# Kernel optimization log

Measured on AMD Instinct MI355X. Metric: run time of the kernel, lower is better.

The kernel has to match this reference:

```python
import jax, jax.numpy as jnp
import numpy as np
from jax import lax

B, T_IN, T_OUT = 32, 256, 500
N_MEL, ENC_DIM = 80, 512
ATT_RNN, DEC_RNN, PRENET, ATT_DIM = 1024, 1024, 256, 128
LOC_F, LOC_K = 32, 31
P_ATT_DROP, P_DEC_DROP = 0.1, 0.1


def setup_inputs() -> dict:
    key = jax.random.key(0)
    ks = jax.random.split(key, 24)
    rn = lambda k, s, sc=0.02: jax.random.normal(k, s, dtype=jnp.float32) * sc
    inp = {}
    inp['memory'] = jax.random.normal(ks[0], (B, T_IN, ENC_DIM), dtype=jnp.float32)
    inp['decoder_inputs'] = jax.random.normal(ks[1], (B, N_MEL, T_OUT), dtype=jnp.float32)
    inp['memory_lengths'] = jax.random.randint(ks[2], (B,), T_IN // 2, T_IN + 1)
    inp['prenet_w1'] = rn(ks[3], (PRENET, N_MEL))
    inp['prenet_w2'] = rn(ks[4], (PRENET, PRENET))
    inp['att_w_ih'] = rn(ks[5], (4 * ATT_RNN, PRENET + ENC_DIM))
    inp['att_w_hh'] = rn(ks[6], (4 * ATT_RNN, ATT_RNN))
    inp['att_b_ih'] = jnp.zeros((4 * ATT_RNN,), jnp.float32)
    inp['att_b_hh'] = jnp.zeros((4 * ATT_RNN,), jnp.float32)
    inp['query_w'] = rn(ks[7], (ATT_DIM, ATT_RNN))
    inp['memory_w'] = rn(ks[8], (ATT_DIM, ENC_DIM))
    inp['v_w'] = rn(ks[9], (1, ATT_DIM))
    inp['loc_conv_w'] = rn(ks[10], (LOC_F, 2, LOC_K))
    inp['loc_dense_w'] = rn(ks[11], (ATT_DIM, LOC_F))
    inp['dec_w_ih'] = rn(ks[12], (4 * DEC_RNN, ATT_RNN + ENC_DIM))
    inp['dec_w_hh'] = rn(ks[13], (4 * DEC_RNN, DEC_RNN))
    inp['dec_b_ih'] = jnp.zeros((4 * DEC_RNN,), jnp.float32)
    inp['dec_b_hh'] = jnp.zeros((4 * DEC_RNN,), jnp.float32)
    inp['proj_w'] = rn(ks[14], (N_MEL, DEC_RNN + ENC_DIM))
    inp['proj_b'] = jnp.zeros((N_MEL,), jnp.float32)
    inp['gate_w'] = rn(ks[15], (1, DEC_RNN + ENC_DIM))
    inp['gate_b'] = jnp.zeros((1,), jnp.float32)
    return inp


def _lstm_cell(x, h, c, w_ih, w_hh, b_ih, b_hh):
    gates = x @ w_ih.T + b_ih + h @ w_hh.T + b_hh
    i, f, g, o = jnp.split(gates, 4, axis=-1)
    c2 = jax.nn.sigmoid(f) * c + jax.nn.sigmoid(i) * jnp.tanh(g)
    h2 = jax.nn.sigmoid(o) * jnp.tanh(c2)
    return h2, c2


def _dropout_masks():
    # deterministic dropout masks (training=True semantics), keep-prob scaled
    kd = jax.random.key(1)
    k1, k2, k3, k4 = jax.random.split(kd, 4)
    m1 = jax.random.bernoulli(k1, 0.5, (T_OUT + 1, B, PRENET)).astype(jnp.float32) / 0.5
    m2 = jax.random.bernoulli(k2, 0.5, (T_OUT + 1, B, PRENET)).astype(jnp.float32) / 0.5
    ma = jax.random.bernoulli(k3, 1 - P_ATT_DROP, (T_OUT, B, ATT_RNN)).astype(jnp.float32) / (1 - P_ATT_DROP)
    md = jax.random.bernoulli(k4, 1 - P_DEC_DROP, (T_OUT, B, DEC_RNN)).astype(jnp.float32) / (1 - P_DEC_DROP)
    return m1, m2, ma, md


def _decode(memory, decoder_inputs, memory_lengths, prenet_w1, prenet_w2,
            att_w_ih, att_w_hh, att_b_ih, att_b_hh, query_w, memory_w, v_w,
            loc_conv_w, loc_dense_w, dec_w_ih, dec_w_hh, dec_b_ih, dec_b_hh,
            proj_w, proj_b, gate_w, gate_b):
    pm1, pm2, att_drop, dec_drop = _dropout_masks()
    processed_memory = jnp.einsum('bte,ae->bta', memory, memory_w)  # (B,T_in,128)
    pad_mask = jnp.arange(T_IN)[None, :] >= memory_lengths[:, None]  # True = padded

    # teacher-forced decoder inputs: (B,n_mel,T) -> (T,B,n_mel), prepend go frame
    dec_in = jnp.transpose(decoder_inputs, (2, 0, 1))
    dec_in = jnp.concatenate([jnp.zeros((1, B, N_MEL), dec_in.dtype), dec_in], 0)
    # prenet (relu + dropout p=0.5, always training)
    x = jax.nn.relu(dec_in @ prenet_w1.T) * pm1
    x = jax.nn.relu(x @ prenet_w2.T) * pm2
    prenet_out = x[:T_OUT]  # (T,B,256)

    pad = (LOC_K - 1) // 2

    def attention(att_h, aw, aw_cum):
        pq = att_h @ query_w.T  # (B,128)
        awc = jnp.stack([aw, aw_cum], axis=1)  # (B,2,T_in)
        loc = lax.conv_general_dilated(awc, loc_conv_w, (1,), [(pad, pad)],
                                       dimension_numbers=('NCH', 'OIH', 'NCH'))  # (B,32,T_in)
        loc = jnp.einsum('bft,af->bta', loc, loc_dense_w)  # (B,T_in,128)
        energies = jnp.tanh(pq[:, None, :] + loc + processed_memory) @ v_w[0]  # (B,T_in)
        energies = jnp.where(pad_mask, -jnp.inf, energies)
        w = jax.nn.softmax(energies, axis=1)
        ctx = jnp.einsum('bt,bte->be', w, memory)  # (B,512)
        return ctx, w

    def step(carry, xs):
        ah, ac, dh, dc, aw, aw_cum, ctx = carry
        pn, adm, ddm = xs
        cell_in = jnp.concatenate([pn, ctx], axis=-1)  # (B,768)
        ah, ac = _lstm_cell(cell_in, ah, ac, att_w_ih, att_w_hh, att_b_ih, att_b_hh)
        ah = ah * adm
        ctx, aw = attention(ah, aw, aw_cum)
        aw_cum = aw_cum + aw
        din = jnp.concatenate([ah, ctx], axis=-1)  # (B,1536)
        dh, dc = _lstm_cell(din, dh, dc, dec_w_ih, dec_w_hh, dec_b_ih, dec_b_hh)
        dh = dh * ddm
        dhac = jnp.concatenate([dh, ctx], axis=-1)  # (B,1536)
        mel = dhac @ proj_w.T + proj_b  # (B,80)
        gate = (dhac @ gate_w.T + gate_b)[:, 0]  # (B,)
        return (ah, ac, dh, dc, aw, aw_cum, ctx), (mel, gate, aw)

    z = lambda d: jnp.zeros((B, d), jnp.float32)
    init = (z(ATT_RNN), z(ATT_RNN), z(DEC_RNN), z(DEC_RNN),
            jnp.zeros((B, T_IN), jnp.float32), jnp.zeros((B, T_IN), jnp.float32), z(ENC_DIM))
    _, (mels, gates, aligns) = lax.scan(step, init, (prenet_out, att_drop, dec_drop))

    mel_outputs = jnp.transpose(mels, (1, 2, 0))   # (B, n_mel, T_out)
    gate_outputs = gates.T                          # (B, T_out)
    alignments = jnp.transpose(aligns, (1, 0, 2))   # (B, T_out, T_in)
    return mel_outputs, gate_outputs, alignments


def reference(memory, decoder_inputs, memory_lengths, prenet_w1, prenet_w2,
              att_w_ih, att_w_hh, att_b_ih, att_b_hh, query_w, memory_w, v_w,
              loc_conv_w, loc_dense_w, dec_w_ih, dec_w_hh, dec_b_ih, dec_b_hh,
              proj_w, proj_b, gate_w, gate_b):
    return _decode(memory, decoder_inputs, memory_lengths, prenet_w1, prenet_w2,
                   att_w_ih, att_w_hh, att_b_ih, att_b_hh, query_w, memory_w, v_w,
                   loc_conv_w, loc_dense_w, dec_w_ih, dec_w_hh, dec_b_ih, dec_b_hh,
                   proj_w, proj_b, gate_w, gate_b)
```

## Files before the change

kernel.cpp:

```cpp
#include <hip/hip_runtime.h>
#include <math.h>
#include <string.h>

#define TOUT 500
#define AOFF 1296000
#define GOFF 1280000
#define TF_BITS_XOR 1

typedef float f32x4 __attribute__((ext_vector_type(4)));
typedef short bf16x8 __attribute__((ext_vector_type(8)));
typedef unsigned short ushort4_t __attribute__((ext_vector_type(4)));
typedef unsigned u32x4 __attribute__((ext_vector_type(4)));

struct Params {
  const float *memory, *dec_in, *pw1, *pw2, *awih, *awhh, *abih, *abhh;
  const float *qw, *mw, *vw, *lcw, *ldw, *dwih, *dwhh, *dbih, *dbhh;
  const float *pjw, *pjb, *gw, *gb;
  const int* mlen;
  float* out;
  unsigned short *ahb0, *ahb1, *dhb0, *dhb1, *ctxb0, *ctxb1;
  unsigned *slots;
  unsigned *flags;
  float *x1, *w1t, *w2t, *mwt, *ldwt, *ba, *bd;
  unsigned short *pre_bf, *pm_bf, *mem_bf, *qw_bf, *wpa, *wpd;
  unsigned *mma, *mmd, *mm1, *mm2;
};

__host__ __device__ inline void tf_block(unsigned k0, unsigned k1, unsigned x0, unsigned x1,
                                         unsigned& o0, unsigned& o1) {
  unsigned ks2 = k0 ^ k1 ^ 0x1BD11BDAu;
  x0 += k0; x1 += k1;
#define TFR(r) { x0 += x1; x1 = (x1 << r) | (x1 >> (32 - r)); x1 ^= x0; }
  TFR(13) TFR(15) TFR(26) TFR(6)
  x0 += k1;  x1 += ks2 + 1u;
  TFR(17) TFR(29) TFR(16) TFR(24)
  x0 += ks2; x1 += k0 + 2u;
  TFR(13) TFR(15) TFR(26) TFR(6)
  x0 += k0;  x1 += k1 + 3u;
  TFR(17) TFR(29) TFR(16) TFR(24)
  x0 += k1;  x1 += ks2 + 4u;
  TFR(13) TFR(15) TFR(26) TFR(6)
  x0 += ks2; x1 += k0 + 5u;
#undef TFR
  o0 = x0; o1 = x1;
}

__device__ inline float sigf(float x) { return 1.f / (1.f + __expf(-x)); }
__device__ inline float tanh_fast(float x) {
  float ax = fabsf(x);
  float t = __expf(-2.f * ax);
  float r = (1.f - t) / (1.f + t);
  return copysignf(r, x);
}
__device__ inline unsigned short f2bf(float f) {
  unsigned u = __float_as_uint(f);
  unsigned r = (u + 0x7FFFu + ((u >> 16) & 1u)) >> 16;
  return (unsigned short)r;
}
__device__ inline float bf2f(unsigned short u) {
  return __uint_as_float((unsigned)u << 16);
}

__device__ inline unsigned long long ld_coh64(const void* ptr) {
  return __hip_atomic_load((unsigned long long*)ptr, __ATOMIC_RELAXED, __HIP_MEMORY_SCOPE_SYSTEM);
}
__device__ inline unsigned ld_coh32(const unsigned* ptr) {
  return __hip_atomic_load(ptr, __ATOMIC_RELAXED, __HIP_MEMORY_SCOPE_SYSTEM);
}
__device__ inline void st_coh32(unsigned* ptr, unsigned v) {
  __hip_atomic_store(ptr, v, __ATOMIC_RELAXED, __HIP_MEMORY_SCOPE_SYSTEM);
}

template<bool COH>
__device__ __forceinline__ u32x4 ld16(const void* ptr) {
  u32x4 r;
  if constexpr (COH)
    asm volatile("global_load_dwordx4 %0, %1, off sc0 sc1" : "=v"(r) : "v"(ptr));
  else
    asm volatile("global_load_dwordx4 %0, %1, off" : "=v"(r) : "v"(ptr));
  return r;
}

#define LD4(p) (*(const float4*)(p))

__global__ void maskgen_kernel(Params p, unsigned k1a, unsigned k1b, unsigned k2a, unsigned k2b,
                               unsigned k3a, unsigned k3b, unsigned k4a, unsigned k4b) {
  int t = blockIdx.x * 256 + threadIdx.x;
  unsigned ka, kb; unsigned* dst; float pp;
  if (t < 512000)       { ka = k3a; kb = k3b; dst = p.mma; pp = 0.9f; }
  else if (t < 1024000) { t -= 512000;  ka = k4a; kb = k4b; dst = p.mmd; pp = 0.9f; }
  else if (t < 1152256) { t -= 1024000; ka = k1a; kb = k1b; dst = p.mm1; pp = 0.5f; }
  else if (t < 1280512) { t -= 1152256; ka = k2a; kb = k2b; dst = p.mm2; pp = 0.5f; }
  else return;
  unsigned word = 0u;
  for (int i = 0; i < 32; ++i) {
    unsigned o0, o1;
    tf_block(ka, kb, 0u, (unsigned)t * 32u + (unsigned)i, o0, o1);
#if TF_BITS_XOR
    unsigned bits = o0 ^ o1;
#else
    unsigned bits = o0;
#endif
    unsigned fb = (bits >> 9) | 0x3f800000u;
    float u = __uint_as_float(fb) - 1.0f;
    if (u < pp) word |= (1u << i);
  }
  dst[t] = word;
}

__global__ void prep_misc(Params p) {
  int i = blockIdx.x * 256 + threadIdx.x;
  if (i < 20480) { int k = i >> 8, u = i & 255; p.w1t[i] = p.pw1[u * 80 + k]; return; }
  i -= 20480;
  if (i < 65536) { int k = i >> 8, u = i & 255; p.w2t[i] = p.pw2[u * 256 + k]; return; }
  i -= 65536;
  if (i < 65536) { int k = i >> 7, a = i & 127; p.mwt[i] = p.mw[a * 512 + k]; return; }
  i -= 65536;
  if (i < 131072) { p.qw_bf[i] = f2bf(p.qw[i]); return; }
  i -= 131072;
  if (i < 4096) { int f = i >> 7, a = i & 127; p.ldwt[i] = p.ldw[a * 32 + f]; return; }
  i -= 4096;
  if (i < 4096) { int col = (i & 3) * 1024 + (i >> 2); p.ba[i] = p.abih[col] + p.abhh[col]; return; }
  i -= 4096;
  if (i < 4096) { int col = (i & 3) * 1024 + (i >> 2); p.bd[i] = p.dbih[col] + p.dbhh[col]; return; }
  i -= 4096;
  if (i < 4194304) { p.mem_bf[i] = f2bf(p.memory[i]); return; }
}

__global__ void pack_att(Params p) {
  int idx = blockIdx.x * 256 + threadIdx.x;
  if (idx >= 256 * 56 * 64) return;
  int l = idx & 63;
  int c = (idx >> 6) % 56;
  int T = idx / (56 * 64);
  int n = T * 16 + (l & 15);
  int col = (n & 3) * 1024 + (n >> 2);
  int kb = c * 32 + 8 * (l >> 4);
  bf16x8 v;
#pragma unroll
  for (int j = 0; j < 8; ++j) {
    int k = kb + j;
    float f = (k < 768) ? p.awih[(size_t)col * 768 + k] : p.awhh[(size_t)col * 1024 + k - 768];
    v[j] = (short)f2bf(f);
  }
  *(bf16x8*)(p.wpa + (size_t)idx * 8) = v;
}
__global__ void pack_dec(Params p) {
  int idx = blockIdx.x * 256 + threadIdx.x;
  if (idx >= 256 * 80 * 64) return;
  int l = idx & 63;
  int c = (idx >> 6) % 80;
  int T = idx / (80 * 64);
  int n = T * 16 + (l & 15);
  int col = (n & 3) * 1024 + (n >> 2);
  int kb = c * 32 + 8 * (l >> 4);
  bf16x8 v;
#pragma unroll
  for (int j = 0; j < 8; ++j) {
    int k = kb + j;
    float f = (k < 1536) ? p.dwih[(size_t)col * 1536 + k] : p.dwhh[(size_t)col * 1024 + k - 1536];
    v[j] = (short)f2bf(f);
  }
  *(bf16x8*)(p.wpd + (size_t)idx * 8) = v;
}

__global__ void prenet1_kernel(Params p) {
  __shared__ float din[8][80];
  int wg = blockIdx.x, tid = threadIdx.x;
  int r0 = wg * 8;
  for (int idx = tid; idx < 8 * 80; idx += 256) {
    int j = idx / 80, kk = idx % 80;
    int r = r0 + j; int t = r >> 5, b = r & 31;
    din[j][kk] = (t == 0) ? 0.f : p.dec_in[(size_t)b * 40000 + (size_t)kk * 500 + (t - 1)];
  }
  __syncthreads();
  float acc[8] = {0,0,0,0,0,0,0,0};
  for (int k = 0; k < 80; ++k) {
    float wv = p.w1t[k * 256 + tid];
#pragma unroll
    for (int j = 0; j < 8; ++j) acc[j] += din[j][k] * wv;
  }
  for (int j = 0; j < 8; ++j) {
    int r = r0 + j;
    unsigned e = (unsigned)r * 256u + tid;
    float mv = ((p.mm1[e >> 5] >> (e & 31)) & 1u) ? 2.0f : 0.0f;
    p.x1[(size_t)r * 256 + tid] = fmaxf(acc[j], 0.f) * mv;
  }
}
__global__ void prenet2_kernel(Params p) {
  __shared__ float rows[8][256];
  int wg = blockIdx.x, tid = threadIdx.x;
  int r0 = wg * 8;
  for (int idx = tid; idx < 8 * 256; idx += 256) {
    int j = idx >> 8, kk = idx & 255;
    rows[j][kk] = p.x1[(size_t)(r0 + j) * 256 + kk];
  }
  __syncthreads();
  float acc[8] = {0,0,0,0,0,0,0,0};
  for (int k = 0; k < 256; ++k) {
    float wv = p.w2t[k * 256 + tid];
#pragma unroll
    for (int j = 0; j < 8; ++j) acc[j] += rows[j][k] * wv;
  }
  for (int j = 0; j < 8; ++j) {
    int r = r0 + j;
    unsigned e = (unsigned)r * 256u + tid;
    float mv = ((p.mm2[e >> 5] >> (e & 31)) & 1u) ? 2.0f : 0.0f;
    p.pre_bf[(size_t)r * 256 + tid] = f2bf(fmaxf(acc[j], 0.f) * mv);
  }
}

__global__ void pm_kernel(Params p) {
  __shared__ float mrows[16][512];
  int wg = blockIdx.x;
  int b = wg >> 4, tc = wg & 15;
  int tid = threadIdx.x;
  int t0 = tc * 16;
  for (int idx = tid; idx < 16 * 512; idx += 128) {
    int i = idx >> 9, k = idx & 511;
    mrows[i][k] = p.memory[((size_t)b * 256 + t0 + i) * 512 + k];
  }
  __syncthreads();
  float acc[16];
#pragma unroll
  for (int i = 0; i < 16; ++i) acc[i] = 0.f;
  for (int k = 0; k < 512; ++k) {
    float wv = p.mwt[k * 128 + tid];
#pragma unroll
    for (int i = 0; i < 16; ++i) acc[i] += mrows[i][k] * wv;
  }
  for (int i = 0; i < 16; ++i)
    p.pm_bf[((size_t)b * 256 + t0 + i) * 128 + tid] = f2bf(acc[i]);
}

template<int LEN, bool COH>
struct Seg {
  static constexpr int CPR = LEN / 8;
  static constexpr int N = (32 * CPR) / 512;
  u32x4 r[N];
  __device__ __forceinline__ void load(const unsigned short* src, int srcStride, int tid) {
#pragma unroll
    for (int i = 0; i < N; ++i) {
      int idx = tid + i * 512;
      int b = idx / CPR, c = idx % CPR;
      r[i] = ld16<COH>(src + (size_t)b * srcStride + c * 8);
    }
  }
  __device__ __forceinline__ void store(unsigned short* dst, int dstOff, int dstStride, int tid) {
#pragma unroll
    for (int i = 0; i < N; ++i) {
      int idx = tid + i * 512;
      int b = idx / CPR, c = idx % CPR;
      *(u32x4*)(dst + b * dstStride + dstOff + c * 8) = r[i];
    }
  }
};

__device__ __forceinline__ void drain_vm() {
  asm volatile("s_waitcnt vmcnt(0)" ::: "memory");
  __builtin_amdgcn_sched_barrier(0);
}

#define MFMA_BF16(a, b, c) __builtin_amdgcn_mfma_f32_16x16x32_bf16(a, b, c, 0, 0, 0)

template<int NC, int CPW, int P0J, bool ATT>
__device__ __forceinline__ void gemm_tile2(const Params& p, const bf16x8* bfa, const bf16x8* bfb,
                                           int lane, int v, int s,
                                           const unsigned short* ctxb_prev,
                                           const unsigned short* ahb_prev,
                                           const unsigned short* dhb_prev2,
                                           unsigned short* Abuf, float* pl, int tid) {
  const int arow = lane & 15;
  const int kgrp = (lane >> 4) * 8;
  f32x4 acc00 = {0,0,0,0}, acc01 = {0,0,0,0}, acc10 = {0,0,0,0}, acc11 = {0,0,0,0};

  const int RS0 = ATT ? 776 : 1288;
  if (ATT) {
    Seg<256, false> s0; Seg<512, true> s1;
    s0.load(p.pre_bf + (size_t)s * 32 * 256, 256, tid);
    s1.load(ctxb_prev, 512, tid);
    drain_vm();
    s0.store(Abuf, 0, RS0, tid);
    s1.store(Abuf, 256, RS0, tid);
  } else {
    Seg<1024, true> s0; Seg<256, true> s1;
    s0.load(ahb_prev, 1024, tid);
    s1.load(ctxb_prev, 512, tid);
    drain_vm();
    s0.store(Abuf, 0, RS0, tid);
    s1.store(Abuf, 1024, RS0, tid);
  }
  __syncthreads();
#pragma unroll
  for (int j = 0; j < P0J; ++j) {
    const int kc = (v + 8 * j) * 32;
    const int off = arow * RS0 + kc + kgrp;
    bf16x8 a0 = *(const bf16x8*)&Abuf[off];
    bf16x8 a1 = *(const bf16x8*)&Abuf[off + 16 * RS0];
    acc00 = MFMA_BF16(a0, bfa[j], acc00);
    acc01 = MFMA_BF16(a1, bfa[j], acc01);
    acc10 = MFMA_BF16(a0, bfb[j], acc10);
    acc11 = MFMA_BF16(a1, bfb[j], acc11);
  }
  __syncthreads();

  const int RS1 = ATT ? 1032 : 1288;
  if (ATT) {
    Seg<1024, true> s0;
    s0.load(ahb_prev, 1024, tid);
    drain_vm();
    s0.store(Abuf, 0, RS1, tid);
  } else {
    Seg<256, true> s0; Seg<1024, true> s1;
    s0.load(ctxb_prev + 256, 512, tid);
    s1.load(dhb_prev2, 1024, tid);
    drain_vm();
    s0.store(Abuf, 0, RS1, tid);
    s1.store(Abuf, 256, RS1, tid);
  }
  __syncthreads();
  const int K1 = ATT ? 768 : 1280;
#pragma unroll
  for (int j = P0J; j < CPW; ++j) {
    const int kc = (v + 8 * j) * 32 - K1;
    const int off = arow * RS1 + kc + kgrp;
    bf16x8 a0 = *(const bf16x8*)&Abuf[off];
    bf16x8 a1 = *(const bf16x8*)&Abuf[off + 16 * RS1];
    acc00 = MFMA_BF16(a0, bfa[j], acc00);
    acc01 = MFMA_BF16(a1, bfa[j], acc01);
    acc10 = MFMA_BF16(a0, bfb[j], acc10);
    acc11 = MFMA_BF16(a1, bfb[j], acc11);
  }
  __syncthreads();

  const int po = (lane & 15) * 17 + (lane >> 4) * 4;
#pragma unroll
  for (int j = 0; j < 4; ++j) {
    pl[v * 1088 +   0 + po + j] = acc00[j];
    pl[v * 1088 + 272 + po + j] = acc01[j];
    pl[v * 1088 + 544 + po + j] = acc10[j];
    pl[v * 1088 + 816 + po + j] = acc11[j];
  }
}

template<bool MASTER>
__device__ __forceinline__ void gbar(const Params& p, int wg, int tid, unsigned bargen) {
  __syncthreads();
  if (MASTER) {
    if (tid == 0) st_coh32(p.slots + wg * 32, bargen);
    for (;;) {
      int ok = 1;
      if (tid < 256) ok = (ld_coh32(p.slots + tid * 32) >= bargen) ? 1 : 0;
      if (__syncthreads_count(ok) == 512) break;
      __builtin_amdgcn_s_sleep(1);
    }
    if (tid < 8) st_coh32(p.flags + tid * 32, bargen);
  } else {
    if (tid == 0) {
      st_coh32(p.slots + wg * 32, bargen);
      while (ld_coh32(p.flags + (wg & 7) * 32) < bargen)
        __builtin_amdgcn_s_sleep(2);
    }
    __syncthreads();
  }
}

template<bool IS_ATT, bool MASTER>
__device__ __forceinline__ void run_scan(const Params& p, int wg, int tid,
                                         unsigned short* Abuf, float* pl, float* gates,
                                         float* cst, float* aw_l, float* awc_l, float* sm,
                                         unsigned short* ahst, unsigned short* cxst,
                                         unsigned short* hst) {
  const int lane = tid & 63;
  const int v = tid >> 6;
  constexpr int NC  = IS_ATT ? 56 : 80;
  constexpr int CPW = IS_ATT ? 7 : 10;
  constexpr int P0J = IS_ATT ? 3 : 5;
  const int wgl = IS_ATT ? wg : (wg - 128);
  const int Tb  = wgl * 2;

  bf16x8 bfa[CPW], bfb[CPW];
  {
    const unsigned short* wp = IS_ATT ? p.wpa : p.wpd;
#pragma unroll
    for (int j = 0; j < CPW; ++j) {
      const int c = v + 8 * j;
      const unsigned short* bp = wp + ((size_t)(Tb * NC + c) * 64 + lane) * 8;
      bfa[j] = *(const bf16x8*)bp;
      bfb[j] = *(const bf16x8*)(bp + (size_t)NC * 64 * 8);
    }
  }

  unsigned bargen = 0;

  for (int s = 0; s <= 500; ++s) {
    const int sb = s & 1;
    const unsigned short* ahb_prev  = sb ? p.ahb0 : p.ahb1;
    unsigned short*       ahb_cur   = sb ? p.ahb1 : p.ahb0;
    const unsigned short* dhb_prev2 = sb ? p.dhb1 : p.dhb0;
    unsigned short*       dhb_out   = sb ? p.dhb0 : p.dhb1;
    const unsigned short* ctxb_prev = sb ? p.ctxb0 : p.ctxb1;
    unsigned short*       ctxb_cur  = sb ? p.ctxb1 : p.ctxb0;

    const bool gemm_on = IS_ATT ? (s < 500) : (s >= 1);

    if (gemm_on)
      gemm_tile2<NC, CPW, P0J, IS_ATT>(p, bfa, bfb, lane, v, s, ctxb_prev, ahb_prev, dhb_prev2, Abuf, pl, tid);
    __syncthreads();
    if (gemm_on) {
      const float* bias = IS_ATT ? p.ba : p.bd;
      const int nb32 = wgl * 32;
#pragma unroll
      for (int rep = 0; rep < 2; ++rep) {
        int o = rep * 512 + tid;
        int tile = o >> 9, half = (o >> 8) & 1, n = (o >> 4) & 15, brow = o & 15;
        int o2 = (tile * 2 + half) * 272 + n * 17 + brow;
        float acc = 0.f;
#pragma unroll
        for (int w = 0; w < 8; ++w) acc += pl[w * 1088 + o2];
        int n_local = tile * 16 + n;
        gates[n_local * 33 + half * 16 + brow] = acc + bias[nb32 + n_local];
      }
    }
    __syncthreads();
    if (gemm_on && tid < 256) {
      int u_local = tid >> 5, b = tid & 31;
      float gi = gates[(u_local * 4 + 0) * 33 + b];
      float gf = gates[(u_local * 4 + 1) * 33 + b];
      float gg = gates[(u_local * 4 + 2) * 33 + b];
      float go = gates[(u_local * 4 + 3) * 33 + b];
      float I = sigf(gi), F = sigf(gf), G = tanh_fast(gg), O = sigf(go);
      float c2 = F * cst[tid] + I * G;
      float h = O * tanh_fast(c2);
      cst[tid] = c2;
      int u = wgl * 8 + u_local;
      float mv;
      if (IS_ATT) {
        unsigned e = ((unsigned)s * 32 + b) * 1024u + u;
        mv = ((p.mma[e >> 5] >> (e & 31)) & 1u) ? (1.f / 0.9f) : 0.f;
      } else {
        unsigned e = ((unsigned)(s - 1) * 32 + b) * 1024u + u;
        mv = ((p.mmd[e >> 5] >> (e & 31)) & 1u) ? (1.f / 0.9f) : 0.f;
      }
      hst[tid] = f2bf(h * mv);
    }
    __syncthreads();
    if (gemm_on && tid < 128) {
      int j = tid >> 5, bb = tid & 31;
      unsigned lo = hst[j * 64 + bb], hi = hst[j * 64 + 32 + bb];
      unsigned val = lo | (hi << 16);
      unsigned short* basep = IS_ATT ? ahb_cur : dhb_out;
      int T8 = wgl * 8;
      st_coh32((unsigned*)(basep + (size_t)bb * 1024 + T8 + 2 * j), val);
    }

    gbar<MASTER>(p, wg, tid, ++bargen);

    if (IS_ATT && wg < 32) {
      if (s < 500) {
        const int b = wg;
        unsigned short* locT_bf = (unsigned short*)pl;
        float* ldwt_l = (float*)((char*)(void*)pl + 16640);
        {
          const float4* srcw = (const float4*)p.ldwt;
          float4* dstw = (float4*)ldwt_l;
          dstw[tid] = srcw[tid];
          dstw[tid + 512] = srcw[tid + 512];
        }
        if (tid < 256) {
          unsigned long long q = ld_coh64((const unsigned long long*)(ahb_cur + (size_t)b * 1024) + tid);
          *(unsigned long long*)&ahst[tid * 4] = q;
        }
#pragma unroll
        for (int rep = 0; rep < 4; ++rep) {
          int qd = rep * 512 + tid;
          int f = qd >> 6, tq = (qd & 63) * 4;
          const float* wf = p.lcw + f * 62;
          float w[36]; float acc[4] = {0, 0, 0, 0};
#pragma unroll
          for (int j2 = 0; j2 < 9; ++j2) {
            float4 x = *(const float4*)&aw_l[tq + j2 * 4];
            w[j2*4] = x.x; w[j2*4+1] = x.y; w[j2*4+2] = x.z; w[j2*4+3] = x.w;
          }
#pragma unroll
          for (int k = 0; k < 31; ++k) {
            float cc = wf[k];
            acc[0] += w[k+1]*cc; acc[1] += w[k+2]*cc; acc[2] += w[k+3]*cc; acc[3] += w[k+4]*cc;
          }
#pragma unroll
          for (int j2 = 0; j2 < 9; ++j2) {
            float4 x = *(const float4*)&awc_l[tq + j2 * 4];
            w[j2*4] = x.x; w[j2*4+1] = x.y; w[j2*4+2] = x.z; w[j2*4+3] = x.w;
          }
#pragma unroll
          for (int k = 0; k < 31; ++k) {
            float cc = wf[31 + k];
            acc[0] += w[k+1]*cc; acc[1] += w[k+2]*cc; acc[2] += w[k+3]*cc; acc[3] += w[k+4]*cc;
          }
#pragma unroll
          for (int j2 = 0; j2 < 4; ++j2) locT_bf[f * 260 + tq + j2] = f2bf(acc[j2]);
        }
        __syncthreads();
        {
          int a = tid & 127, kq = tid >> 7;
          const unsigned short* qp = p.qw_bf + (size_t)a * 1024 + kq * 256;
          float acc = 0.f;
#pragma unroll 4
          for (int j = 0; j < 256; j += 8) {
            bf16x8 qv = *(const bf16x8*)(qp + j);
            bf16x8 av = *(const bf16x8*)&ahst[kq * 256 + j];
#pragma unroll
            for (int j2 = 0; j2 < 8; ++j2)
              acc += bf2f((unsigned short)av[j2]) * bf2f((unsigned short)qv[j2]);
          }
          sm[256 + kq * 128 + a] = acc;
          if (tid < 128) sm[128 + tid] = p.vw[tid];
        }
        __syncthreads();
        if (tid < 128) sm[tid] = sm[256 + tid] + sm[384 + tid] + sm[512 + tid] + sm[640 + tid];
        __syncthreads();
        {
          int t = tid & 255, h2 = tid >> 8;
          float lt[32];
#pragma unroll
          for (int f = 0; f < 32; ++f) lt[f] = bf2f(locT_bf[f * 260 + t]);
          const unsigned short* pmp = p.pm_bf + ((size_t)b * 256 + t) * 128;
          float e = 0.f;
#pragma unroll 2
          for (int ac = 0; ac < 16; ++ac) {
            int a0 = h2 * 64 + ac * 4;
            float4 l2 = {0, 0, 0, 0};
#pragma unroll
            for (int f = 0; f < 32; ++f) {
              float4 wv = *(const float4*)&ldwt_l[f * 128 + a0];
              l2.x += lt[f]*wv.x; l2.y += lt[f]*wv.y; l2.z += lt[f]*wv.z; l2.w += lt[f]*wv.w;
            }
            ushort4_t pv = *(const ushort4_t*)(pmp + a0);
            e += tanh_fast(sm[a0+0] + l2.x + bf2f(pv.x)) * sm[128+a0+0];
            e += tanh_fast(sm[a0+1] + l2.y + bf2f(pv.y)) * sm[128+a0+1];
            e += tanh_fast(sm[a0+2] + l2.z + bf2f(pv.z)) * sm[128+a0+2];
            e += tanh_fast(sm[a0+3] + l2.w + bf2f(pv.w)) * sm[128+a0+3];
          }
          sm[256 + h2 * 256 + t] = e;
        }
        __syncthreads();
        if (tid < 256) {
          float en = sm[256 + tid] + sm[512 + tid];
          float w = (tid < p.mlen[b]) ? __expf(en) : 0.f;
          sm[768 + tid] = w;
        }
        __syncthreads();
        if (tid < 32) {
          float sub = 0.f;
#pragma unroll
          for (int i = 0; i < 8; ++i) sub += sm[768 + tid * 8 + i];
          sm[256 + tid] = sub;
        }
        __syncthreads();
        if (tid == 0) {
          float S = 0.f;
#pragma unroll
          for (int i = 0; i < 32; ++i) S += sm[256 + i];
          sm[1281] = 1.f / S;
        }
        __syncthreads();
        if (tid < 256) {
          float awv = sm[768 + tid] * sm[1281];
          aw_l[16 + tid] = awv;
          awc_l[16 + tid] += awv;
          p.out[(size_t)AOFF + (size_t)b * 128000 + (size_t)s * 256 + tid] = awv;
          sm[1024 + tid] = awv;
        }
        __syncthreads();
        {
          const unsigned short* mb = p.mem_bf + (size_t)b * 131072 + tid;
          float acc = 0.f;
#pragma unroll 8
          for (int t2 = 0; t2 < 256; ++t2) acc += sm[1024 + t2] * bf2f(mb[(size_t)t2 * 512]);
          cxst[tid] = f2bf(acc);
        }
        __syncthreads();
        if (tid < 256) {
          unsigned val = (unsigned)cxst[2 * tid] | ((unsigned)cxst[2 * tid + 1] << 16);
          st_coh32((unsigned*)(ctxb_cur + (size_t)b * 512 + 2 * tid), val);
        }
      }
    } else if (wg >= 32) {
      if (s >= 1) {
        int idx = wg - 32;
        int b = idx / 7, c7 = idx % 7;
        int m0 = c7 * 12, mc = (c7 == 6) ? 8 : 12;
        if (tid < 384) {
          unsigned long long q;
          if (tid < 256) q = ld_coh64((const unsigned long long*)(dhb_out + (size_t)b * 1024) + tid);
          else           q = ld_coh64((const unsigned long long*)(ctxb_prev + (size_t)b * 512) + (tid - 256));
          *(unsigned long long*)&ahst[tid * 4] = q;
        }
        __syncthreads();
        int mi = tid >> 5, kg = tid & 31;
        if (mi < mc) {
          int m = m0 + mi;
          const float* pw = p.pjw + (size_t)m * 1536 + kg * 48;
          float acc = 0.f;
#pragma unroll 4
          for (int j = 0; j < 48; ++j) acc += bf2f(ahst[kg * 48 + j]) * pw[j];
          sm[mi * 32 + kg] = acc;
        }
        if (c7 == 6 && tid >= 384) {
          int kg2 = tid - 384;
          const float* gwp = p.gw + kg2 * 12;
          float acc = 0.f;
#pragma unroll
          for (int j = 0; j < 12; ++j) acc += bf2f(ahst[kg2 * 12 + j]) * gwp[j];
          sm[512 + kg2] = acc;
        }
        __syncthreads();
        if (tid < mc) {
          float r = p.pjb[m0 + tid];
#pragma unroll
          for (int j = 0; j < 32; ++j) r += sm[tid * 32 + j];
          p.out[(size_t)b * 40000 + (size_t)(m0 + tid) * 500 + (s - 1)] = r;
        }
        if (c7 == 6 && tid == 384) {
          float r = p.gb[0];
#pragma unroll
          for (int j = 0; j < 128; ++j) r += sm[512 + j];
          p.out[(size_t)GOFF + (size_t)b * 500 + (s - 1)] = r;
        }
      }
    }

    gbar<MASTER>(p, wg, tid, ++bargen);
  }
}

__global__ void __launch_bounds__(512, 2) scan_kernel(Params p) {
  const int wg = blockIdx.x;
  const int tid = threadIdx.x;

  __shared__ __align__(16) unsigned short Abuf[32 * 1288];
  float* pl = (float*)Abuf;
  __shared__ float gates[32 * 33];
  __shared__ float cst[256];
  __shared__ float aw_l[292], awc_l[292];
  __shared__ float sm[1536];
  __shared__ unsigned short ahst[1536];
  __shared__ unsigned short cxst[512];
  __shared__ unsigned short hst[256];

  if (tid < 256) cst[tid] = 0.f;
  if (tid < 292) { aw_l[tid] = 0.f; awc_l[tid] = 0.f; }

  if (wg < 128) {
    if (wg == 32) run_scan<true, true >(p, wg, tid, Abuf, pl, gates, cst, aw_l, awc_l, sm, ahst, cxst, hst);
    else          run_scan<true, false>(p, wg, tid, Abuf, pl, gates, cst, aw_l, awc_l, sm, ahst, cxst, hst);
  } else {
    run_scan<false, false>(p, wg, tid, Abuf, pl, gates, cst, aw_l, awc_l, sm, ahst, cxst, hst);
  }
}

extern "C" void kernel_launch(void* const* d_in, const int* in_sizes, int n_in,
                              void* d_out, int out_size, void* d_ws, size_t ws_size,
                              hipStream_t stream) {
  Params p;
  p.memory = (const float*)d_in[0];
  p.dec_in = (const float*)d_in[1];
  p.mlen   = (const int*)d_in[2];
  p.pw1  = (const float*)d_in[3];
  p.pw2  = (const float*)d_in[4];
  p.awih = (const float*)d_in[5];
  p.awhh = (const float*)d_in[6];
  p.abih = (const float*)d_in[7];
  p.abhh = (const float*)d_in[8];
  p.qw   = (const float*)d_in[9];
  p.mw   = (const float*)d_in[10];
  p.vw   = (const float*)d_in[11];
  p.lcw  = (const float*)d_in[12];
  p.ldw  = (const float*)d_in[13];
  p.dwih = (const float*)d_in[14];
  p.dwhh = (const float*)d_in[15];
  p.dbih = (const float*)d_in[16];
  p.dbhh = (const float*)d_in[17];
  p.pjw  = (const float*)d_in[18];
  p.pjb  = (const float*)d_in[19];
  p.gw   = (const float*)d_in[20];
  p.gb   = (const float*)d_in[21];
  p.out  = (float*)d_out;

  char* cur = (char*)d_ws;
  auto allocf = [&](size_t n) { float* r = (float*)cur; cur += n * sizeof(float); return r; };
  auto allocs = [&](size_t n) { unsigned short* r = (unsigned short*)cur; cur += n * sizeof(unsigned short); return r; };
  p.ahb0 = allocs(32 * 1024); p.ahb1 = allocs(32 * 1024);
  p.dhb0 = allocs(32 * 1024); p.dhb1 = allocs(32 * 1024);
  p.ctxb0 = allocs(32 * 512); p.ctxb1 = allocs(32 * 512);
  p.slots = (unsigned*)cur; cur += 256 * 32 * sizeof(unsigned);
  p.flags = (unsigned*)cur; cur += 8 * 32 * sizeof(unsigned);
  size_t state_bytes = (size_t)(cur - (char*)d_ws);
  p.x1   = allocf((size_t)500 * 32 * 256);
  p.w1t  = allocf(80 * 256);
  p.w2t  = allocf(256 * 256);
  p.mwt  = allocf(512 * 128);
  p.ldwt = allocf(32 * 128);
  p.ba   = allocf(4096);
  p.bd   = allocf(4096);
  p.pre_bf  = allocs((size_t)500 * 32 * 256);
  p.pm_bf   = allocs((size_t)32 * 256 * 128);
  p.mem_bf  = allocs((size_t)32 * 256 * 512);
  p.qw_bf   = allocs(128 * 1024);
  p.wpa     = allocs((size_t)256 * 56 * 64 * 8);
  p.wpd     = allocs((size_t)256 * 80 * 64 * 8);
  p.mma = (unsigned*)cur; cur += 512000u * 4;
  p.mmd = (unsigned*)cur; cur += 512000u * 4;
  p.mm1 = (unsigned*)cur; cur += 128256u * 4;
  p.mm2 = (unsigned*)cur; cur += 128256u * 4;

  (void)hipMemsetAsync(d_ws, 0, state_bytes, stream);

  unsigned k[8];
  {
    unsigned o0, o1;
    tf_block(0u, 1u, 0u, 0u, o0, o1); k[0] = o0; k[1] = o1;
    tf_block(0u, 1u, 0u, 1u, o0, o1); k[2] = o0; k[3] = o1;
    tf_block(0u, 1u, 0u, 2u, o0, o1); k[4] = o0; k[5] = o1;
    tf_block(0u, 1u, 0u, 3u, o0, o1); k[6] = o0; k[7] = o1;
  }

  maskgen_kernel<<<(1280512 + 255) / 256, 256, 0, stream>>>(p, k[0], k[1], k[2], k[3], k[4], k[5], k[6], k[7]);
  prep_misc<<<(4489216 + 255) / 256, 256, 0, stream>>>(p);
  pack_att<<<(917504 + 255) / 256, 256, 0, stream>>>(p);
  pack_dec<<<(1310720 + 255) / 256, 256, 0, stream>>>(p);
  prenet1_kernel<<<2000, 256, 0, stream>>>(p);
  prenet2_kernel<<<2000, 256, 0, stream>>>(p);
  pm_kernel<<<512, 128, 0, stream>>>(p);

  void* args[] = { (void*)&p };
  (void)hipLaunchCooperativeKernel((const void*)scan_kernel, dim3(256), dim3(512), args, 0, stream);
}
```

Baseline: 35.49 ms.

## Transpose bf16 memory for vectorized context loads and cache projection weights in registers

The bf16 encoder memory copy is stored transposed (B, D, T), so the per-step context reduction can read eight contiguous bf16 values per vector load instead of strided scalar loads. The mel-projection weight slice for each thread is loaded once into 48 registers before the time loop instead of being re-read from global memory every step. Launch bounds are relaxed from two blocks per CU to one to make room for the extra registers. In a persistent, grid-barrier-synchronised kernel this raises register pressure and may limit residency of the co-scheduled blocks.

```diff
diff --git a/kernel.cpp b/kernel.cpp
--- a/kernel.cpp
+++ b/kernel.cpp
@@ -22,7 +22,7 @@
   unsigned *slots;
   unsigned *flags;
   float *x1, *w1t, *w2t, *mwt, *ldwt, *ba, *bd;
-  unsigned short *pre_bf, *pm_bf, *mem_bf, *qw_bf, *wpa, *wpd;
+  unsigned short *pre_bf, *pm_bf, *mem_t, *qw_bf, *wpa, *wpd;
   unsigned *mma, *mmd, *mm1, *mm2;
 };
 
@@ -124,7 +124,11 @@
   i -= 4096;
   if (i < 4096) { int col = (i & 3) * 1024 + (i >> 2); p.bd[i] = p.dbih[col] + p.dbhh[col]; return; }
   i -= 4096;
-  if (i < 4194304) { p.mem_bf[i] = f2bf(p.memory[i]); return; }
+  if (i < 4194304) {
+    int b = i >> 17, rem = i & 131071, d = rem >> 8, t = rem & 255;
+    p.mem_t[i] = f2bf(p.memory[((size_t)b * 256 + t) * 512 + d]);
+    return;
+  }
 }
 
 __global__ void pack_att(Params p) {
@@ -388,6 +392,22 @@
       const unsigned short* bp = wp + ((size_t)(Tb * NC + c) * 64 + lane) * 8;
       bfa[j] = *(const bf16x8*)bp;
       bfb[j] = *(const bf16x8*)(bp + (size_t)NC * 64 * 8);
+    }
+  }
+
+  float pjr[48];
+  int melb = 0, melc7 = 0, melm0 = 0, melmc = 0;
+  {
+    if (wg >= 32) {
+      int idx = wg - 32;
+      melb = idx / 7; melc7 = idx % 7;
+      melm0 = melc7 * 12; melmc = (melc7 == 6) ? 8 : 12;
+      int mi = tid >> 5, kg = tid & 31;
+      if (mi < melmc) {
+        const float* pw = p.pjw + (size_t)(melm0 + mi) * 1536 + kg * 48;
+#pragma unroll
+        for (int j = 0; j < 48; ++j) pjr[j] = pw[j];
+      }
     }
   }
 
@@ -573,10 +593,15 @@
         }
         __syncthreads();
         {
-          const unsigned short* mb = p.mem_bf + (size_t)b * 131072 + tid;
+          const unsigned short* mt = p.mem_t + (size_t)b * 131072 + (size_t)tid * 256;
           float acc = 0.f;
 #pragma unroll 8
-          for (int t2 = 0; t2 < 256; ++t2) acc += sm[1024 + t2] * bf2f(mb[(size_t)t2 * 512]);
+          for (int t2 = 0; t2 < 256; t2 += 8) {
+            bf16x8 mv = *(const bf16x8*)(mt + t2);
+#pragma unroll
+            for (int j2 = 0; j2 < 8; ++j2)
+              acc += sm[1024 + t2 + j2] * bf2f((unsigned short)mv[j2]);
+          }
           cxst[tid] = f2bf(acc);
         }
         __syncthreads();
@@ -587,26 +612,21 @@
       }
     } else if (wg >= 32) {
       if (s >= 1) {
-        int idx = wg - 32;
-        int b = idx / 7, c7 = idx % 7;
-        int m0 = c7 * 12, mc = (c7 == 6) ? 8 : 12;
         if (tid < 384) {
           unsigned long long q;
-          if (tid < 256) q = ld_coh64((const unsigned long long*)(dhb_out + (size_t)b * 1024) + tid);
-          else           q = ld_coh64((const unsigned long long*)(ctxb_prev + (size_t)b * 512) + (tid - 256));
+          if (tid < 256) q = ld_coh64((const unsigned long long*)(dhb_out + (size_t)melb * 1024) + tid);
+          else           q = ld_coh64((const unsigned long long*)(ctxb_prev + (size_t)melb * 512) + (tid - 256));
           *(unsigned long long*)&ahst[tid * 4] = q;
         }
         __syncthreads();
         int mi = tid >> 5, kg = tid & 31;
-        if (mi < mc) {
-          int m = m0 + mi;
-          const float* pw = p.pjw + (size_t)m * 1536 + kg * 48;
+        if (mi < melmc) {
           float acc = 0.f;
-#pragma unroll 4
-          for (int j = 0; j < 48; ++j) acc += bf2f(ahst[kg * 48 + j]) * pw[j];
+#pragma unroll
+          for (int j = 0; j < 48; ++j) acc += bf2f(ahst[kg * 48 + j]) * pjr[j];
           sm[mi * 32 + kg] = acc;
         }
-        if (c7 == 6 && tid >= 384) {
+        if (melc7 == 6 && tid >= 384) {
           int kg2 = tid - 384;
           const float* gwp = p.gw + kg2 * 12;
           float acc = 0.f;
@@ -615,17 +635,17 @@
           sm[512 + kg2] = acc;
         }
         __syncthreads();
-        if (tid < mc) {
-          float r = p.pjb[m0 + tid];
+        if (tid < melmc) {
+          float r = p.pjb[melm0 + tid];
 #pragma unroll
           for (int j = 0; j < 32; ++j) r += sm[tid * 32 + j];
-          p.out[(size_t)b * 40000 + (size_t)(m0 + tid) * 500 + (s - 1)] = r;
-        }
-        if (c7 == 6 && tid == 384) {
+          p.out[(size_t)melb * 40000 + (size_t)(melm0 + tid) * 500 + (s - 1)] = r;
+        }
+        if (melc7 == 6 && tid == 384) {
           float r = p.gb[0];
 #pragma unroll
           for (int j = 0; j < 128; ++j) r += sm[512 + j];
-          p.out[(size_t)GOFF + (size_t)b * 500 + (s - 1)] = r;
+          p.out[(size_t)GOFF + (size_t)melb * 500 + (s - 1)] = r;
         }
       }
     }
@@ -634,7 +654,7 @@
   }
 }
 
-__global__ void __launch_bounds__(512, 2) scan_kernel(Params p) {
+__global__ void __launch_bounds__(512, 1) scan_kernel(Params p) {
   const int wg = blockIdx.x;
   const int tid = threadIdx.x;
 
@@ -705,7 +725,7 @@
   p.bd   = allocf(4096);
   p.pre_bf  = allocs((size_t)500 * 32 * 256);
   p.pm_bf   = allocs((size_t)32 * 256 * 128);
-  p.mem_bf  = allocs((size_t)32 * 256 * 512);
+  p.mem_t   = allocs((size_t)32 * 512 * 256);
   p.qw_bf   = allocs(128 * 1024);
   p.wpa     = allocs((size_t)256 * 56 * 64 * 8);
   p.wpd     = allocs((size_t)256 * 80 * 64 * 8);
```

New measurement: 35.82 ms. Within noise of the previous version (+0.9%).
